# Optimization experiments

Measured on AMD Instinct MI355X. Metric: run time of the kernel, lower is better.

The kernel has to match this reference:

```python
import jax, jax.numpy as jnp
import numpy as np

D = 2048   # hidden_d
V = 2048   # hidden_v
L = 512    # number of points in seq
P = 64     # len(positions); decode steps = P + 1 (final special-symbol step)


def setup_inputs() -> dict:
    key = jax.random.key(0)
    ks = jax.random.split(key, 10)
    s = 0.02  # init scale for weights
    return dict(
        initial_state=jax.random.normal(ks[0], (1, D), dtype=jnp.float32),
        encoder_states=jax.random.normal(ks[1], (L + 1, D), dtype=jnp.float32),
        seq_points=jax.random.normal(ks[2], (L, 3), dtype=jnp.float32),
        positions=jax.random.randint(ks[3], (P,), 0, L),
        # LSTMCell params (torch layout: gates ordered i,f,g,o)
        W_ih=jax.random.normal(ks[4], (4 * D, 3), dtype=jnp.float32) * s,
        W_hh=jax.random.normal(ks[5], (4 * D, D), dtype=jnp.float32) * s,
        b_ih=jnp.zeros((4 * D,), dtype=jnp.float32),
        b_hh=jnp.zeros((4 * D,), dtype=jnp.float32),
        # Pointer params
        We_w=jax.random.normal(ks[6], (V, D), dtype=jnp.float32) * s,
        We_b=jnp.zeros((V,), dtype=jnp.float32),
        Wd_w=jax.random.normal(ks[7], (V, D), dtype=jnp.float32) * s,
        Wd_b=jnp.zeros((V,), dtype=jnp.float32),
        v_w=jax.random.normal(ks[8], (1, V), dtype=jnp.float32) * s,
        v_b=jnp.zeros((1,), dtype=jnp.float32),
    )


def reference(initial_state, encoder_states, seq_points, positions,
              W_ih, W_hh, b_ih, b_hh, We_w, We_b, Wd_w, Wd_b, v_w, v_b):
    """Teacher-forced pointer-network decode (positions given).

    Returns (logits [T, L+1], hidden_states [T, D], losses [T]) with
    T = len(positions) + 1 (final step targets the special symbol).
    """
    special = jnp.array([0.0, 0.0, 1.0], dtype=seq_points.dtype)
    stack_seq = jnp.concatenate([seq_points, special[None]], axis=0)  # [L+1, 3]
    Lseq = seq_points.shape[0]

    # teacher-forced inputs: step 0 = special symbol, step t = seq[positions[t-1]]
    xs = jnp.concatenate([special[None], stack_seq[positions]], axis=0)  # [T, 3]
    targets = jnp.concatenate([positions, jnp.array([Lseq])], axis=0)    # [T]

    # encoder projection is step-invariant: hoist out of the loop
    enc_proj = encoder_states @ We_w.T + We_b  # [L+1, V]

    h0 = initial_state[0]            # [D]
    c0 = jnp.zeros_like(h0)

    def step(carry, inp):
        h, c = carry
        x, tgt = inp
        gates = W_ih @ x + b_ih + W_hh @ h + b_hh  # [4D]
        i, f, g, o = jnp.split(gates, 4)
        i = jax.nn.sigmoid(i)
        f = jax.nn.sigmoid(f)
        g = jnp.tanh(g)
        o = jax.nn.sigmoid(o)
        c = f * c + i * g
        h = o * jnp.tanh(c)
        t = jnp.tanh(enc_proj + Wd_w @ h + Wd_b)   # [L+1, V]
        logits = t @ v_w[0] + v_b[0]               # [L+1]
        # CrossEntropyLoss on [1, L+1] logits with class target tgt
        loss = jax.nn.logsumexp(logits) - logits[tgt]
        return (h, c), (logits, h, loss)

    _, (logits, hs, losses) = jax.lax.scan(step, (h0, c0), (xs, targets))
    return logits, hs, losses
```

## Files before the change

### kernel.cpp

```cpp
#include <hip/hip_runtime.h>

typedef unsigned int uint32;
typedef unsigned short u16;

#define DD    2048
#define LP1   513
#define TT    65
#define FOURD 8192
#define NWG   256
#define SLOTW 32
#define PSTR  5

typedef __attribute__((ext_vector_type(8))) short short8;
typedef __attribute__((ext_vector_type(4))) float f32x4;

__device__ __forceinline__ float frcp(float x) { return __builtin_amdgcn_rcpf(x); }
__device__ __forceinline__ float sigm(float x) {
    return frcp(1.f + exp2f(-1.4426950408889634f * x));
}
__device__ __forceinline__ float tanh_fast(float x) {
    float e = exp2f(2.8853900817779268f * x);
    return fmaf(-2.f, frcp(1.f + e), 1.f);
}
__device__ __forceinline__ float bflo(uint32 w) {
    union { uint32 i; float f; } c; c.i = w << 16; return c.f;
}
__device__ __forceinline__ float bfhi(uint32 w) {
    union { uint32 i; float f; } c; c.i = w & 0xffff0000u; return c.f;
}
__device__ __forceinline__ uint32 f2bf(float f) {
    union { float f; uint32 i; } c; c.f = f;
    return (c.i + 0x7fffu + ((c.i >> 16) & 1u)) >> 16;
}
__device__ __forceinline__ uint32 pack2(float a, float b) {
    return f2bf(a) | (f2bf(b) << 16);
}

#if __has_builtin(__builtin_amdgcn_fdot2_f32_bf16)
#define HAVE_DOT2 1
typedef __attribute__((ext_vector_type(2))) __bf16 bf16x2;
__device__ __forceinline__ float dot2bf(uint32 a, uint32 b, float c) {
    union { uint32 u; bf16x2 v; } x, y; x.u = a; y.u = b;
    return __builtin_amdgcn_fdot2_f32_bf16(x.v, y.v, c, false);
}
#endif

__global__ __launch_bounds__(256) void conv_bf16_kernel(
    const float* __restrict__ src, u16* __restrict__ dst)
{
    size_t i = ((size_t)blockIdx.x * 256 + threadIdx.x) * 8;
    float4 a = *(const float4*)(src + i);
    float4 b = *(const float4*)(src + i + 4);
    uint4 o;
    o.x = pack2(a.x, a.y); o.y = pack2(a.z, a.w);
    o.z = pack2(b.x, b.y); o.w = pack2(b.z, b.w);
    *(uint4*)(dst + i) = o;
}

__global__ __launch_bounds__(256) void xg_kernel(
    const float* __restrict__ W_ih, const float* __restrict__ b_ih,
    const float* __restrict__ b_hh, const float* __restrict__ seq,
    const int* __restrict__ pos, float* __restrict__ xg,
    uint32* __restrict__ hX)
{
    if (blockIdx.y < 2)
        hX[blockIdx.y * 8192 + blockIdx.x * 256 + threadIdx.x] = 0u;
    int t = blockIdx.y;
    int r = blockIdx.x * 256 + threadIdx.x;
    float x0, x1, x2;
    if (t == 0) { x0 = 0.f; x1 = 0.f; x2 = 1.f; }
    else {
        int p = pos[t - 1];
        x0 = seq[p * 3 + 0]; x1 = seq[p * 3 + 1]; x2 = seq[p * 3 + 2];
    }
    float acc = b_ih[r] + b_hh[r];
    acc = fmaf(W_ih[r * 3 + 0], x0, acc);
    acc = fmaf(W_ih[r * 3 + 1], x1, acc);
    acc = fmaf(W_ih[r * 3 + 2], x2, acc);
    xg[(size_t)t * FOURD + r] = acc;
}

#define GLSTR 72
__global__ __launch_bounds__(256) void gemm_bf16_kernel(
    const u16* __restrict__ A, const u16* __restrict__ B,
    const float* __restrict__ bias, float* __restrict__ C,
    int M, int N, int K)
{
    __shared__ u16 As[64 * GLSTR];
    __shared__ u16 Bs[64 * GLSTR];
    int tid = threadIdx.x;
    int wave = tid >> 6, lane = tid & 63;
    int m0 = blockIdx.y * 64, n0 = blockIdx.x * 64;
    int wm = (wave >> 1) * 32, wn = (wave & 1) * 32;
    int srow = tid >> 2, scol = (tid & 3) * 16;

    f32x4 acc[2][2] = {};
    int fr = lane & 15, fq = (lane >> 4) * 8;
    int am = m0 + srow;
    const uint4* ap = (const uint4*)(A + (size_t)am * K + scol);
    const uint4* bp = (const uint4*)(B + (size_t)(n0 + srow) * K + scol);

    uint4 a0 = {0,0,0,0}, a1 = a0, b0, b1;
    if (am < M) { a0 = ap[0]; a1 = ap[1]; }
    b0 = bp[0]; b1 = bp[1];

    for (int k0 = 0; k0 < K; k0 += 64) {
        __syncthreads();
        {
            uint4* ad = (uint4*)(As + srow * GLSTR + scol);
            ad[0] = a0; ad[1] = a1;
            uint4* bd = (uint4*)(Bs + srow * GLSTR + scol);
            bd[0] = b0; bd[1] = b1;
        }
        __syncthreads();

        if (k0 + 64 < K) {
            int off = (k0 + 64) >> 3;
            if (am < M) { a0 = ap[off]; a1 = ap[off + 1]; }
            b0 = bp[off]; b1 = bp[off + 1];
        }

        #pragma unroll
        for (int kk = 0; kk < 64; kk += 32) {
            short8 af0 = *(const short8*)(As + (wm + fr) * GLSTR + kk + fq);
            short8 af1 = *(const short8*)(As + (wm + 16 + fr) * GLSTR + kk + fq);
            short8 bf0 = *(const short8*)(Bs + (wn + fr) * GLSTR + kk + fq);
            short8 bf1 = *(const short8*)(Bs + (wn + 16 + fr) * GLSTR + kk + fq);
            acc[0][0] = __builtin_amdgcn_mfma_f32_16x16x32_bf16(af0, bf0, acc[0][0], 0, 0, 0);
            acc[0][1] = __builtin_amdgcn_mfma_f32_16x16x32_bf16(af0, bf1, acc[0][1], 0, 0, 0);
            acc[1][0] = __builtin_amdgcn_mfma_f32_16x16x32_bf16(af1, bf0, acc[1][0], 0, 0, 0);
            acc[1][1] = __builtin_amdgcn_mfma_f32_16x16x32_bf16(af1, bf1, acc[1][1], 0, 0, 0);
        }
    }

    int cn = lane & 15, cr = (lane >> 4) * 4;
    #pragma unroll
    for (int i = 0; i < 2; i++) {
        #pragma unroll
        for (int r = 0; r < 4; r++) {
            int m = m0 + wm + i * 16 + cr + r;
            if (m < M) {
                #pragma unroll
                for (int j = 0; j < 2; j++) {
                    int n = n0 + wn + j * 16 + cn;
                    C[(size_t)m * N + n] = acc[i][j][r] + bias[n];
                }
            }
        }
    }
}

#define SMEM_FUSED (32 * 2048 * 2 + TT * 32 * 4 + TT * 8 * 4 + NWG * PSTR * 4)

__global__ __launch_bounds__(256, 1) void lstm_fused_kernel(
    const float* __restrict__ Whh, const float* __restrict__ init_h,
    const float* __restrict__ xg, uint32* __restrict__ hX,
    float* __restrict__ outH, u16* __restrict__ Hb)
{
    extern __shared__ char smem[];
    u16*    Ws   = (u16*)smem;
    float*  xg_s = (float*)(smem + 32 * 2048 * 2);
    float*  ho_s = xg_s + TT * 32;
    uint32* hp_s = (uint32*)(ho_s + TT * 8);

    int tid = threadIdx.x;
    int b = blockIdx.x;
    int wave = tid >> 6, lane = tid & 63;
    int jj = lane & 1;
    int dl = 2 * wave + jj;

    #pragma unroll 4
    for (int r = 0; r < 32; r++) {
        int g = r >> 3, j = r & 7;
        const float4* s4 =
            (const float4*)(Whh + ((size_t)(g * DD + 8 * b + j)) * DD) + tid * 2;
        float4 x = s4[0], y = s4[1];
        uint4 o;
        o.x = pack2(x.x, x.y); o.y = pack2(x.z, x.w);
        o.z = pack2(y.x, y.y); o.w = pack2(y.z, y.w);
        *(uint4*)(Ws + r * DD + tid * 8) = o;
    }
    for (int idx = tid; idx < TT * 32; idx += 256) {
        int t = idx >> 5, rr = idx & 31, g = rr >> 3, j = rr & 7;
        xg_s[idx] = xg[(size_t)t * FOURD + g * DD + 8 * b + j];
    }
    __syncthreads();

    const uint4* Wq = (const uint4*)Ws;
    float cst = 0.f;

    for (int t = 0; t < TT; t++) {
        uint32 hp[4][4];
        if (t == 0) {
            #pragma unroll
            for (int i = 0; i < 4; i++) {
                const float4* p = (const float4*)(init_h + i * 512 + lane * 8);
                float4 x = p[0], y = p[1];
                hp[i][0] = pack2(x.x, x.y); hp[i][1] = pack2(x.z, x.w);
                hp[i][2] = pack2(y.x, y.y); hp[i][3] = pack2(y.z, y.w);
            }
        } else {
            const uint32* gs =
                hX + ((size_t)(((t - 1) & 1) * NWG + tid)) * SLOTW;
            uint32 gv[8];
            #pragma unroll
            for (int j = 0; j < 8; j++)
                gv[j] = __hip_atomic_load(gs + j, __ATOMIC_RELAXED,
                                          __HIP_MEMORY_SCOPE_AGENT);
            for (;;) {
                bool ok = true;
                #pragma unroll
                for (int j = 0; j < 8; j++) ok &= ((gv[j] >> 16) >= (uint32)t);
                if (ok) break;
                __builtin_amdgcn_s_sleep(1);
                #pragma unroll
                for (int j = 0; j < 8; j++)
                    if ((gv[j] >> 16) < (uint32)t)
                        gv[j] = __hip_atomic_load(gs + j, __ATOMIC_RELAXED,
                                                  __HIP_MEMORY_SCOPE_AGENT);
            }
            hp_s[tid * PSTR + 0] = (gv[0] & 0xffffu) | (gv[1] << 16);
            hp_s[tid * PSTR + 1] = (gv[2] & 0xffffu) | (gv[3] << 16);
            hp_s[tid * PSTR + 2] = (gv[4] & 0xffffu) | (gv[5] << 16);
            hp_s[tid * PSTR + 3] = (gv[6] & 0xffffu) | (gv[7] << 16);
            __syncthreads();

            #pragma unroll
            for (int i = 0; i < 4; i++) {
                const uint32* sl = hp_s + (i * 64 + lane) * PSTR;
                hp[i][0] = sl[0]; hp[i][1] = sl[1];
                hp[i][2] = sl[2]; hp[i][3] = sl[3];
            }
        }

        float a[4][2];
        #pragma unroll
        for (int g = 0; g < 4; g++)
            #pragma unroll
            for (int q = 0; q < 2; q++) {
                int r = g * 8 + 2 * wave + q;
                float s = 0.f;
                #pragma unroll
                for (int i = 0; i < 4; i++) {
                    uint4 ww = Wq[r * 256 + i * 64 + lane];
#ifdef HAVE_DOT2
                    s = dot2bf(ww.x, hp[i][0], s);
                    s = dot2bf(ww.y, hp[i][1], s);
                    s = dot2bf(ww.z, hp[i][2], s);
                    s = dot2bf(ww.w, hp[i][3], s);
#else
                    s = fmaf(bflo(ww.x), bflo(hp[i][0]), s);
                    s = fmaf(bfhi(ww.x), bfhi(hp[i][0]), s);
                    s = fmaf(bflo(ww.y), bflo(hp[i][1]), s);
                    s = fmaf(bfhi(ww.y), bfhi(hp[i][1]), s);
                    s = fmaf(bflo(ww.z), bflo(hp[i][2]), s);
                    s = fmaf(bfhi(ww.z), bfhi(hp[i][2]), s);
                    s = fmaf(bflo(ww.w), bflo(hp[i][3]), s);
                    s = fmaf(bfhi(ww.w), bfhi(hp[i][3]), s);
#endif
                }
                a[g][q] = s;
            }

        #pragma unroll
        for (int off = 1; off < 64; off <<= 1) {
            #pragma unroll
            for (int g = 0; g < 4; g++) {
                a[g][0] += __shfl_xor(a[g][0], off);
                a[g][1] += __shfl_xor(a[g][1], off);
            }
        }
        float si = jj ? a[0][1] : a[0][0];
        float sf = jj ? a[1][1] : a[1][0];
        float sg = jj ? a[2][1] : a[2][0];
        float so = jj ? a[3][1] : a[3][0];
        int xb = t * 32;
        si += xg_s[xb + dl];      sf += xg_s[xb + 8 + dl];
        sg += xg_s[xb + 16 + dl]; so += xg_s[xb + 24 + dl];
        float ig = sigm(si), fg = sigm(sf), gg = tanh_fast(sg), og = sigm(so);
        cst = fmaf(fg, cst, ig * gg);
        float hh = og * tanh_fast(cst);
        if (lane < 2) {
            uint32 wrd = ((uint32)(t + 1) << 16) | f2bf(hh);
            __hip_atomic_store(
                &hX[((size_t)((t & 1) * NWG + b)) * SLOTW + dl], wrd,
                __ATOMIC_RELAXED, __HIP_MEMORY_SCOPE_AGENT);
            ho_s[t * 8 + dl] = hh;
        }
        if (t > 0) __syncthreads();
    }

    __syncthreads();
    for (int idx = tid; idx < TT * 8; idx += 256) {
        int t = idx >> 3, j = idx & 7;
        float hv_ = ho_s[idx];
        outH[(size_t)t * DD + 8 * b + j] = hv_;
        Hb[(size_t)t * DD + 8 * b + j] = (u16)f2bf(hv_);
    }
}

__global__ __launch_bounds__(256) void ptr_kernel(
    const float* __restrict__ enc_proj, const float* __restrict__ Dm,
    const float* __restrict__ vw, const float* __restrict__ vb,
    float* __restrict__ outL)
{
    __shared__ float vw_s[DD];
    __shared__ float Dm_s[DD];
    __shared__ float enc_s[4][DD];
    int tid = threadIdx.x;
    int l0 = blockIdx.x * 4;
    int t0 = blockIdx.y * 33;
    int nt = blockIdx.y ? 32 : 33;

    ((float4*)vw_s)[tid] = ((const float4*)vw)[tid];
    ((float4*)vw_s)[tid + 256] = ((const float4*)vw)[tid + 256];
    #pragma unroll
    for (int r = 0; r < 4; r++) {
        int l = l0 + r;
        if (l < LP1) {
            const float4* ep = (const float4*)(enc_proj + (size_t)l * DD);
            ((float4*)enc_s[r])[tid] = ep[tid];
            ((float4*)enc_s[r])[tid + 256] = ep[tid + 256];
        }
    }
    int wave = tid >> 6, lane = tid & 63;
    float vbf = vb[0];

    for (int tt = 0; tt < nt; tt++) {
        int t = t0 + tt;
        __syncthreads();
        const float4* dp = (const float4*)(Dm + (size_t)t * DD);
        ((float4*)Dm_s)[tid] = dp[tid];
        ((float4*)Dm_s)[tid + 256] = dp[tid + 256];
        __syncthreads();

        int l = l0 + wave;
        if (l < LP1) {
            const float* er = enc_s[wave];
            float acc = 0.f;
            #pragma unroll 8
            for (int i2 = 0; i2 < 32; i2++) {
                int v = lane + (i2 << 6);
                acc = fmaf(vw_s[v], tanh_fast(er[v] + Dm_s[v]), acc);
            }
            #pragma unroll
            for (int off = 1; off < 64; off <<= 1)
                acc += __shfl_xor(acc, off);
            if (lane == 0)
                outL[(size_t)t * LP1 + l] = acc + vbf;
        }
    }
}

__global__ __launch_bounds__(256) void loss_kernel(
    const float* __restrict__ LG, const int* __restrict__ pos,
    float* __restrict__ outLoss)
{
    int t = blockIdx.x, tid = threadIdx.x;
    __shared__ float red[256];
    const float* row = LG + (size_t)t * LP1;

    float m = -3.4e38f;
    for (int i = tid; i < LP1; i += 256) m = fmaxf(m, row[i]);
    red[tid] = m; __syncthreads();
    for (int s = 128; s > 0; s >>= 1) {
        if (tid < s) red[tid] = fmaxf(red[tid], red[tid + s]);
        __syncthreads();
    }
    float mx = red[0]; __syncthreads();

    float sum = 0.f;
    for (int i = tid; i < LP1; i += 256)
        sum += exp2f((row[i] - mx) * 1.4426950408889634f);
    red[tid] = sum; __syncthreads();
    for (int s = 128; s > 0; s >>= 1) {
        if (tid < s) red[tid] += red[tid + s];
        __syncthreads();
    }
    if (tid == 0) {
        int tgt = (t < TT - 1) ? pos[t] : (LP1 - 1);
        float lse = mx + 0.6931471805599453f * log2f(red[0]);
        outLoss[t] = lse - row[tgt];
    }
}

extern "C" void kernel_launch(void* const* d_in, const int* in_sizes, int n_in,
                              void* d_out, int out_size, void* d_ws, size_t ws_size,
                              hipStream_t stream) {
    const float* init_h = (const float*)d_in[0];
    const float* enc    = (const float*)d_in[1];
    const float* seq    = (const float*)d_in[2];
    const int*   pos    = (const int*)d_in[3];
    const float* W_ih   = (const float*)d_in[4];
    const float* W_hh   = (const float*)d_in[5];
    const float* b_ih   = (const float*)d_in[6];
    const float* b_hh   = (const float*)d_in[7];
    const float* We_w   = (const float*)d_in[8];
    const float* We_b   = (const float*)d_in[9];
    const float* Wd_w   = (const float*)d_in[10];
    const float* Wd_b   = (const float*)d_in[11];
    const float* v_w    = (const float*)d_in[12];
    const float* v_b    = (const float*)d_in[13];
    float* out = (float*)d_out;

    float* outL    = out;
    float* outH    = out + (size_t)TT * LP1;
    float* outLoss = outH + (size_t)TT * DD;

    float* ws = (float*)d_ws;
    float* enc_proj = ws;
    float* xg       = enc_proj + (size_t)LP1 * DD;
    float* Dm       = xg + (size_t)TT * FOURD;
    uint32* hX      = (uint32*)(Dm + (size_t)TT * DD);
    u16* enc_b = (u16*)(hX + 2 * NWG * SLOTW);
    u16* Web   = enc_b + (size_t)LP1 * DD;
    u16* Wdb   = Web + (size_t)DD * DD;
    u16* Hb    = Wdb + (size_t)DD * DD;

    static bool attr_done = false;
    if (!attr_done) {
        (void)hipFuncSetAttribute((const void*)lstm_fused_kernel,
                                  hipFuncAttributeMaxDynamicSharedMemorySize,
                                  SMEM_FUSED);
        attr_done = true;
    }

    conv_bf16_kernel<<<dim3(513), 256, 0, stream>>>(enc, enc_b);
    conv_bf16_kernel<<<dim3(2048), 256, 0, stream>>>(We_w, Web);
    conv_bf16_kernel<<<dim3(2048), 256, 0, stream>>>(Wd_w, Wdb);

    xg_kernel<<<dim3(32, TT), 256, 0, stream>>>(W_ih, b_ih, b_hh, seq, pos, xg,
                                                hX);

    gemm_bf16_kernel<<<dim3(32, 9), 256, 0, stream>>>(enc_b, Web, We_b, enc_proj,
                                                      LP1, DD, DD);

    {
        const float* whh = W_hh; const float* ih = init_h; const float* xgp = xg;
        uint32* hx = hX; float* oh = outH; u16* hbb = Hb;
        void* kargs[] = { (void*)&whh, (void*)&ih, (void*)&xgp, (void*)&hx,
                          (void*)&oh, (void*)&hbb };
        hipError_t e = hipLaunchCooperativeKernel(
            (const void*)lstm_fused_kernel, dim3(NWG), dim3(256),
            kargs, SMEM_FUSED, stream);
        if (e != hipSuccess) {
            (void)hipGetLastError();
            lstm_fused_kernel<<<dim3(NWG), dim3(256), SMEM_FUSED, stream>>>(
                W_hh, init_h, xg, hX, outH, Hb);
        }
    }

    gemm_bf16_kernel<<<dim3(32, 2), 256, 0, stream>>>(Hb, Wdb, Wd_b, Dm,
                                                      TT, DD, DD);

    ptr_kernel<<<dim3(129, 2), 256, 0, stream>>>(enc_proj, Dm, v_w, v_b, outL);

    loss_kernel<<<TT, 256, 0, stream>>>(outL, pos, outLoss);
}
```

Measured before the change: 633.0 us.

## Replace per-step workgroup barriers with flag-tagged double-buffered LDS exchange

The per-step exchange of hidden-state words through shared memory now uses a double-buffered LDS area holding the raw tagged words (step number in the upper 16 bits). Consumers spin on workgroup-scope atomic loads until the tags show the current step, which lets both __syncthreads calls inside the recurrence loop be dropped. The goal is to cut barrier latency on the serial 65-step critical path. The cost is more LDS traffic (eight words per slot instead of four packed ones) and spin loops, and correctness now depends on the tag ordering and the double buffering preventing overwrites.

```diff
diff --git a/kernel.cpp b/kernel.cpp
--- a/kernel.cpp
+++ b/kernel.cpp
@@ -9,7 +9,7 @@
 #define FOURD 8192
 #define NWG   256
 #define SLOTW 32
-#define PSTR  5
+#define LREL  9
 
 typedef __attribute__((ext_vector_type(8))) short short8;
 typedef __attribute__((ext_vector_type(4))) float f32x4;
@@ -150,7 +150,7 @@
     }
 }
 
-#define SMEM_FUSED (32 * 2048 * 2 + TT * 32 * 4 + TT * 8 * 4 + NWG * PSTR * 4)
+#define SMEM_FUSED (32 * 2048 * 2 + TT * 32 * 4 + TT * 8 * 4 + 2 * NWG * LREL * 4)
 
 __global__ __launch_bounds__(256, 1) void lstm_fused_kernel(
     const float* __restrict__ Whh, const float* __restrict__ init_h,
@@ -169,6 +169,7 @@
     int jj = lane & 1;
     int dl = 2 * wave + jj;
 
+    for (int idx = tid; idx < 2 * NWG * LREL; idx += 256) hp_s[idx] = 0u;
     #pragma unroll 4
     for (int r = 0; r < 32; r++) {
         int g = r >> 3, j = r & 7;
@@ -215,21 +216,39 @@
                 __builtin_amdgcn_s_sleep(1);
                 #pragma unroll
                 for (int j = 0; j < 8; j++)
-                    if ((gv[j] >> 16) < (uint32)t)
-                        gv[j] = __hip_atomic_load(gs + j, __ATOMIC_RELAXED,
-                                                  __HIP_MEMORY_SCOPE_AGENT);
-            }
-            hp_s[tid * PSTR + 0] = (gv[0] & 0xffffu) | (gv[1] << 16);
-            hp_s[tid * PSTR + 1] = (gv[2] & 0xffffu) | (gv[3] << 16);
-            hp_s[tid * PSTR + 2] = (gv[4] & 0xffffu) | (gv[5] << 16);
-            hp_s[tid * PSTR + 3] = (gv[6] & 0xffffu) | (gv[7] << 16);
-            __syncthreads();
+                    gv[j] = __hip_atomic_load(gs + j, __ATOMIC_RELAXED,
+                                              __HIP_MEMORY_SCOPE_AGENT);
+            }
+            uint32* lb = hp_s + (t & 1) * (NWG * LREL);
+            #pragma unroll
+            for (int j = 0; j < 8; j++)
+                __hip_atomic_store(lb + tid * LREL + j, gv[j],
+                                   __ATOMIC_RELAXED,
+                                   __HIP_MEMORY_SCOPE_WORKGROUP);
 
             #pragma unroll
             for (int i = 0; i < 4; i++) {
-                const uint32* sl = hp_s + (i * 64 + lane) * PSTR;
-                hp[i][0] = sl[0]; hp[i][1] = sl[1];
-                hp[i][2] = sl[2]; hp[i][3] = sl[3];
+                const uint32* sl = lb + (i * 64 + lane) * LREL;
+                uint32 hv[8];
+                #pragma unroll
+                for (int j = 0; j < 8; j++)
+                    hv[j] = __hip_atomic_load(sl + j, __ATOMIC_RELAXED,
+                                              __HIP_MEMORY_SCOPE_WORKGROUP);
+                for (;;) {
+                    bool ok = true;
+                    #pragma unroll
+                    for (int j = 0; j < 8; j++)
+                        ok &= ((hv[j] >> 16) >= (uint32)t);
+                    if (ok) break;
+                    #pragma unroll
+                    for (int j = 0; j < 8; j++)
+                        hv[j] = __hip_atomic_load(sl + j, __ATOMIC_RELAXED,
+                                                  __HIP_MEMORY_SCOPE_WORKGROUP);
+                }
+                hp[i][0] = (hv[0] & 0xffffu) | (hv[1] << 16);
+                hp[i][1] = (hv[2] & 0xffffu) | (hv[3] << 16);
+                hp[i][2] = (hv[4] & 0xffffu) | (hv[5] << 16);
+                hp[i][3] = (hv[6] & 0xffffu) | (hv[7] << 16);
             }
         }
 
@@ -287,7 +306,6 @@
                 __ATOMIC_RELAXED, __HIP_MEMORY_SCOPE_AGENT);
             ho_s[t * 8 + dl] = hh;
         }
-        if (t > 0) __syncthreads();
     }
 
     __syncthreads();
```

New measurement: 903.6 us. +42.8%, slower.
